# Optimization experiments

Measured on AMD Instinct MI355X. Metric: run time of the kernel, lower is better.

## Reference

```python
import jax, jax.numpy as jnp
import numpy as np

B, L, D = 2, 2048, 2048
HQ, HKV = 32, 8
HD = D // HQ  # 64
ROPE_BASE = 10000.0
ROPE_SCALE = 1.0


def setup_inputs() -> dict:
    key = jax.random.key(0)
    ks = jax.random.split(key, 5)
    s = 0.02
    return {
        "x": jax.random.normal(ks[0], (B, L, D), dtype=jnp.float32),
        "pos_ids": jnp.arange(L, dtype=jnp.int64) if jax.config.jax_enable_x64 else jnp.arange(L, dtype=jnp.int32),
        "wq": jax.random.normal(ks[1], (D, D), dtype=jnp.float32) * s,
        "wk": jax.random.normal(ks[2], (HKV * HD, D), dtype=jnp.float32) * s,
        "wv": jax.random.normal(ks[3], (HKV * HD, D), dtype=jnp.float32) * s,
        "wo": jax.random.normal(ks[4], (D, D), dtype=jnp.float32) * s,
    }


def _rope_cos_sin(pos_ids, rot_dim, dtype):
    half = rot_dim // 2
    idx = jnp.arange(half, dtype=jnp.float32)
    inv_freq = (1.0 / (ROPE_BASE ** (idx / half))) * ROPE_SCALE  # [half]
    freqs = pos_ids.astype(dtype)[:, None] * inv_freq.astype(dtype)[None, :]  # [L, half]
    return jnp.cos(freqs), jnp.sin(freqs)


def _apply_rotary(x, cos, sin):
    # x: [B, L, H, Hd]; interleaved pair rotation on full head dim
    b, l, h, hd = x.shape
    xp = x.reshape(b, l, h, hd // 2, 2)
    x1, x2 = xp[..., 0], xp[..., 1]
    c = cos.reshape(1, l, 1, hd // 2)
    s = sin.reshape(1, l, 1, hd // 2)
    y1 = x1 * c - x2 * s
    y2 = x1 * s + x2 * c
    return jnp.stack([y1, y2], axis=-1).reshape(b, l, h, hd)


def reference(x, pos_ids, wq, wk, wv, wo):
    b, l, d = x.shape
    q = (x @ wq.T).reshape(b, l, HQ, HD)
    k = (x @ wk.T).reshape(b, l, HKV, HD)
    v = (x @ wv.T).reshape(b, l, HKV, HD)

    cos, sin = _rope_cos_sin(pos_ids, HD, x.dtype)
    q = _apply_rotary(q, cos, sin)
    k = _apply_rotary(k, cos, sin)

    group = HQ // HKV  # GQA: each kv head serves `group` consecutive q heads
    k = jnp.repeat(k, group, axis=2)  # [b, l, HQ, HD]
    v = jnp.repeat(v, group, axis=2)

    scale = 1.0 / jnp.sqrt(jnp.asarray(HD, dtype=x.dtype))
    scores = jnp.einsum("bqhd,bkhd->bhqk", q, k) * scale  # [b, HQ, l, l]
    causal = jnp.tril(jnp.ones((l, l), dtype=bool))
    neg = jnp.asarray(jnp.finfo(x.dtype).min, dtype=x.dtype)
    scores = jnp.where(causal[None, None], scores, neg)
    attn = jax.nn.softmax(scores, axis=-1)
    out = jnp.einsum("bhqk,bkhd->bqhd", attn, v).reshape(b, l, d)
    return out @ wo.T
```

## Files before the change

### kernel.cpp

```cpp
#include <hip/hip_runtime.h>
#include <stdint.h>

typedef unsigned short u16;
typedef unsigned int   u32;
typedef __bf16 bf16_t;
typedef bf16_t bf16x8 __attribute__((ext_vector_type(8)));
typedef u16    u16x8  __attribute__((ext_vector_type(8)));
typedef float  f32x4  __attribute__((ext_vector_type(4)));
typedef float  f32x16 __attribute__((ext_vector_type(16)));

#define NB   2
#define NL   2048
#define ND   2048
#define NHQ  32
#define NHKV 8
#define NHD  64
#define NQKV 3072
#define QSCALE 0.18033688011112042f
#define SM_SHIFT 24.0f

__device__ __forceinline__ u16 f2bf(float x){
  union{float f;u32 u;} v; v.f = x;
  u32 r = v.u + 0x7FFFu + ((v.u >> 16) & 1u);
  return (u16)(r >> 16);
}
__device__ __forceinline__ float bf2f(u16 b){
  union{u32 u;float f;} v; v.u = ((u32)b) << 16; return v.f;
}

__device__ __forceinline__ float exp2_hw(float x){
#if __has_builtin(__builtin_amdgcn_exp2f)
  return __builtin_amdgcn_exp2f(x);
#else
  float r; asm("v_exp_f32 %0, %1" : "=v"(r) : "v"(x)); return r;
#endif
}

__device__ __forceinline__ void gload_lds16(const void* g, void* l){
  auto gp = reinterpret_cast<__attribute__((address_space(1))) u16*>(
      (uintptr_t)g);
  auto lp = reinterpret_cast<__attribute__((address_space(3))) u16*>(
      (uintptr_t)l);
  __builtin_amdgcn_global_load_lds(gp, lp, 16, 0, 0);
}

__device__ __forceinline__ f32x4 mfma16(bf16x8 a, bf16x8 b, f32x4 c){
  return __builtin_amdgcn_mfma_f32_16x16x32_bf16(a, b, c, 0, 0, 0);
}
__device__ __forceinline__ f32x16 mfma32(bf16x8 a, bf16x8 b, f32x16 c){
  return __builtin_amdgcn_mfma_f32_32x32x16_bf16(a, b, c, 0, 0, 0);
}
__device__ __forceinline__ u32 cvtpk(float lo, float hi){
  u32 w;
  asm("v_cvt_pk_bf16_f32 %0, %1, %2" : "=v"(w) : "v"(lo), "v"(hi));
  return w;
}

template<int N> __device__ __forceinline__ void lgkm_wait(){
  if      constexpr (N == 0)  asm volatile("s_waitcnt lgkmcnt(0)"  ::: "memory");
  else if constexpr (N == 4)  asm volatile("s_waitcnt lgkmcnt(4)"  ::: "memory");
  else if constexpr (N == 8)  asm volatile("s_waitcnt lgkmcnt(8)"  ::: "memory");
  else if constexpr (N == 12) asm volatile("s_waitcnt lgkmcnt(12)" ::: "memory");
  else if constexpr (N == 14) asm volatile("s_waitcnt lgkmcnt(14)" ::: "memory");
  else                        asm volatile("s_waitcnt lgkmcnt(15)" ::: "memory");
  __builtin_amdgcn_sched_barrier(0);
}

#define CV_S1 2097152
#define CV_S2 3145728
#define CV_S3 3407872
#define CV_S4 3670016
#define CV_S5 4718592
#define CV_TOT (CV_S5 + 65536)

__global__ void k_prep(const float* __restrict__ x,  const float* __restrict__ wq,
                       const float* __restrict__ wk, const float* __restrict__ wv,
                       const float* __restrict__ wo, const int* __restrict__ pos,
                       u16* __restrict__ xb, u16* __restrict__ wqkvb, u16* __restrict__ wob,
                       float* __restrict__ cosT, float* __restrict__ sinT){
  int i = blockIdx.x * 256 + threadIdx.x;
  if (i < CV_S5){
    const float4* src; ushort4* dst; int off;
    if (i < CV_S1)      { src = (const float4*)x;  dst = (ushort4*)xb;    off = i; }
    else if (i < CV_S2) { src = (const float4*)wq; dst = (ushort4*)wqkvb; off = i - CV_S1; }
    else if (i < CV_S3) { src = (const float4*)wk; dst = (ushort4*)wqkvb + 1048576; off = i - CV_S2; }
    else if (i < CV_S4) { src = (const float4*)wv; dst = (ushort4*)wqkvb + 1310720; off = i - CV_S3; }
    else                { src = (const float4*)wo; dst = (ushort4*)wob;   off = i - CV_S4; }
    float4 f = src[off];
    ushort4 o;
    o.x = f2bf(f.x); o.y = f2bf(f.y); o.z = f2bf(f.z); o.w = f2bf(f.w);
    dst[off] = o;
  } else {
    int idx = i - CV_S5;
    int l = idx >> 5, k = idx & 31;
    float p = (float)pos[l];
    float inv = __expf(-((float)k * (1.0f/32.0f)) * 9.210340371976184f);
    float fr = p * inv;
    cosT[idx] = cosf(fr);
    sinT[idx] = sinf(fr);
  }
}

template<int BM, int BN, int WRITE_F32>
__global__ __launch_bounds__(512) void k_gemm9(const u16* __restrict__ A,
                                               const u16* __restrict__ Bm,
                                               void* __restrict__ Cp,
                                               int M, int N, int K){
  constexpr int LA_N = BM/64;
  constexpr int LB_N = BN/64;
  constexpr int LN   = LA_N + LB_N;
  constexpr int MR   = BM/32;
  constexpr int MH   = MR/2;
  constexpr int NF   = BN/64;
  __shared__ u16 LAb[2][BM*64];
  __shared__ u16 LBb[2][BN*64];
  const int tid = threadIdx.x;
  const int lane = tid & 63, w = tid >> 6;
  const int wr = w >> 2, wc = w & 3;
  const int lr = lane & 15, lg = lane >> 4;
  const int tn = blockIdx.x * BN, tm = blockIdx.y * BM;
  const size_t Kb = (size_t)K * 2;
  const char* Ab = (const char*)A;
  const char* Bb = (const char*)Bm;

  u32 soff[LN]; int ldoff[LN];
#pragma unroll
  for (int l = 0; l < LN; ++l){
    int o = ((l < LA_N) ? l : (l - LA_N))*8192 + tid*16;
    int s = o ^ (((o>>7)&7)<<4);
    int row = s >> 7, col = s & 127;
    int trow = (l < LA_N) ? (tm + row) : (tn + row);
    soff[l]  = (u32)((size_t)trow * Kb + col);
    ldoff[l] = o;
  }
  const int c0 = ( lg      ^ (lr & 7)) << 4;
  const int c1 = ((4 + lg) ^ (lr & 7)) << 4;
  const int arow = (wr*(BM/2) + lr) * 128;
  const int brow = (wc*(BN/4) + lr) * 128;

  f32x4 acc[MR][NF] = {};
  bf16x8 bfA[NF][2], bfB[NF][2], afA[MH][2], afB[MH][2];
  const int NT = K >> 6;

#pragma unroll
  for (int l = 0; l < LN; ++l){
    char* base = (l < LA_N) ? (char*)LAb[0] : (char*)LBb[0];
    const char* gb = (l < LA_N) ? Ab : Bb;
    gload_lds16(gb + soff[l], base + ldoff[l]);
  }
  asm volatile("s_waitcnt vmcnt(0)" ::: "memory");
  __builtin_amdgcn_s_barrier();
#pragma unroll
  for (int n = 0; n < NF; ++n){
    bfA[n][0] = *(const bf16x8*)((const char*)LBb[0] + brow + n*2048 + c0);
    bfA[n][1] = *(const bf16x8*)((const char*)LBb[0] + brow + n*2048 + c1);
  }
#pragma unroll
  for (int q = 0; q < MH; ++q){
    afA[q][0] = *(const bf16x8*)((const char*)LAb[0] + arow + q*2048 + c0);
    afA[q][1] = *(const bf16x8*)((const char*)LAb[0] + arow + q*2048 + c1);
  }

#define TILE(laC, laN, lbN, bfc, bfn, PRE, KOFF)                            \
    {                                                                       \
                            \
      _Pragma("unroll")                                                     \
      for (int q = 0; q < MH; ++q){                                         \
        afB[q][0] = *(const bf16x8*)((const char*)(laC) + arow + (MH+q)*2048 + c0); \
        afB[q][1] = *(const bf16x8*)((const char*)(laC) + arow + (MH+q)*2048 + c1); \
      }                                                                     \
      if (PRE){                                                             \
        _Pragma("unroll")                                                   \
        for (int l = 0; l < LN; ++l){                                       \
          char* nb_ = (l < LA_N) ? (char*)(laN) : (char*)(lbN);             \
          const char* gb_ = (l < LA_N) ? Ab : Bb;                           \
          gload_lds16(gb_ + soff[l] + (KOFF), nb_ + ldoff[l]);              \
        }                                                                   \
      }                                                                     \
      lgkm_wait<2*MH>();                                                    \
      __builtin_amdgcn_s_setprio(1);                                        \
      _Pragma("unroll")                                                     \
      for (int q = 0; q < MH; ++q){                                         \
        _Pragma("unroll")                                                   \
        for (int n = 0; n < NF; ++n){                                       \
          acc[q][n] = mfma16(afA[q][0], bfc[n][0], acc[q][n]);              \
          acc[q][n] = mfma16(afA[q][1], bfc[n][1], acc[q][n]);              \
        }                                                                   \
      }                                                                     \
      __builtin_amdgcn_s_setprio(0);                                        \
      asm volatile("s_waitcnt vmcnt(0)" ::: "memory");                      \
      __builtin_amdgcn_s_barrier();                                         \
                        \
      if (PRE){                                                             \
        _Pragma("unroll")                                                   \
        for (int n = 0; n < NF; ++n){                                       \
          bfn[n][0] = *(const bf16x8*)((const char*)(lbN) + brow + n*2048 + c0); \
          bfn[n][1] = *(const bf16x8*)((const char*)(lbN) + brow + n*2048 + c1); \
        }                                                                   \
        _Pragma("unroll")                                                   \
        for (int q = 0; q < MH; ++q){                                       \
          afA[q][0] = *(const bf16x8*)((const char*)(laN) + arow + q*2048 + c0); \
          afA[q][1] = *(const bf16x8*)((const char*)(laN) + arow + q*2048 + c1); \
        }                                                                   \
        lgkm_wait<2*NF + 2*MH>();                                           \
      } else {                                                              \
        lgkm_wait<0>();                                                     \
      }                                                                     \
      __builtin_amdgcn_s_setprio(1);                                        \
      _Pragma("unroll")                                                     \
      for (int q = 0; q < MH; ++q){                                         \
        _Pragma("unroll")                                                   \
        for (int n = 0; n < NF; ++n){                                       \
          acc[MH+q][n] = mfma16(afB[q][0], bfc[n][0], acc[MH+q][n]);        \
          acc[MH+q][n] = mfma16(afB[q][1], bfc[n][1], acc[MH+q][n]);        \
        }                                                                   \
      }                                                                     \
      __builtin_amdgcn_s_setprio(0);                                        \
      __builtin_amdgcn_s_barrier();                                         \
    }

#pragma unroll 1
  for (int kt = 0; kt < NT; kt += 2){
    const bool pre1 = (kt + 2 < NT);
    TILE(LAb[0], LAb[1], LBb[1], bfA, bfB, true, (u32)(kt+1)*128)
    TILE(LAb[1], LAb[0], LBb[0], bfB, bfA, pre1, (u32)(kt+2)*128)
  }
#undef TILE

  const int rb = tm + wr*(BM/2) + lg*4;
  const int cb = tn + wc*(BN/4) + lr;
#pragma unroll
  for (int m = 0; m < MR; ++m){
#pragma unroll
    for (int n = 0; n < NF; ++n){
#pragma unroll
      for (int r = 0; r < 4; ++r){
        size_t off = (size_t)(rb + m*16 + r) * N + (cb + n*16);
        if (WRITE_F32) ((float*)Cp)[off] = acc[m][n][r];
        else           ((u16*)Cp)[off]   = f2bf(acc[m][n][r]);
      }
    }
  }
}

__global__ void k_rope_scatter(const u16* __restrict__ qkv, const float* __restrict__ cosT,
                               const float* __restrict__ sinT,
                               u16* __restrict__ Q, u16* __restrict__ Ko, u16* __restrict__ V){
  const int row = blockIdx.x;
  const int b = row >> 11, l = row & 2047;
  const int t = threadIdx.x;
#pragma unroll
  for (int it = 0; it < 6; ++it){
    int pp = t + it*256;
    u32 xin = *reinterpret_cast<const u32*>(&qkv[(size_t)row*NQKV + pp*2]);
    float x1 = bf2f((u16)(xin & 0xFFFFu));
    float x2 = bf2f((u16)(xin >> 16));
    if (pp < 1280){
      int i = pp & 31;
      float c = cosT[l*32 + i], s = sinT[l*32 + i];
      float y1 = x1*c - x2*s;
      float y2 = x1*s + x2*c;
      if (pp < 1024){
        int hh = pp >> 5, d = (pp & 31)*2;
        u32 o = (u32)f2bf(y1*QSCALE) | ((u32)f2bf(y2*QSCALE) << 16);
        *reinterpret_cast<u32*>(&Q[(((size_t)(b*NHQ + hh))*NL + l)*NHD + d]) = o;
      } else {
        int idx = pp - 1024, kvh = idx >> 5, d = (idx & 31)*2;
        u32 o = (u32)f2bf(y1) | ((u32)f2bf(y2) << 16);
        *reinterpret_cast<u32*>(&Ko[(((size_t)(b*NHKV + kvh))*NL + l)*NHD + d]) = o;
      }
    } else {
      int idx = pp - 1280, kvh = idx >> 5, d = (idx & 31)*2;
      *reinterpret_cast<u32*>(&V[(((size_t)(b*NHKV + kvh))*NL + l)*NHD + d]) = xin;
    }
  }
}

__global__ __launch_bounds__(256) void k_transpose(const u16* __restrict__ V, u16* __restrict__ VT){
  __shared__ u16 T[64*72];
  const int bid = blockIdx.x;
  const int slice = bid >> 5, tile = bid & 31;
  const u16* src = V  + (size_t)slice*NL*NHD + (size_t)tile*64*NHD;
  u16*       dst = VT + (size_t)slice*NHD*NL + (size_t)tile*64;
  const int t = threadIdx.x;
  {
    int r = t >> 2, c0 = (t & 3)*16;
    const u16x8* s = reinterpret_cast<const u16x8*>(src + (size_t)r*NHD + c0);
    *reinterpret_cast<u16x8*>(&T[r*72 + c0])     = s[0];
    *reinterpret_cast<u16x8*>(&T[r*72 + c0 + 8]) = s[1];
  }
  __syncthreads();
  {
    int d = t >> 2, l0 = (t & 3)*16;
    u16x8 v0, v1;
#pragma unroll
    for (int j = 0; j < 8; ++j) v0[j] = T[(l0+j)*72 + d];
#pragma unroll
    for (int j = 0; j < 8; ++j) v1[j] = T[(l0+8+j)*72 + d];
    u16* dp = dst + (size_t)d*NL + l0;
    *reinterpret_cast<u16x8*>(dp)     = v0;
    *reinterpret_cast<u16x8*>(dp + 8) = v1;
  }
}

__device__ __forceinline__ void stage_kv32(const u16* __restrict__ Kp, const u16* __restrict__ VTp,
                                           int kvb, u16* lk, u16* lv, int w, int lane){
  const char* ks = (const char*)(Kp + (size_t)kvb*NHD);
  const char* vs = (const char*)VTp + (size_t)kvb*2;
  const int o = w*1024 + lane*16;
  const int swk = o ^ (((o>>7)&7)<<4);
  gload_lds16(ks + swk, (char*)lk + w*1024);
  const int row = o >> 6, c = o & 63;
  gload_lds16(vs + (size_t)row*(NL*2) + (c ^ (((row>>1)&3)<<4)), (char*)lv + w*1024);
}
__device__ __forceinline__ bf16x8 ldsK(const u16* base, int row, int colb){
  return *reinterpret_cast<const bf16x8*>((const char*)base + row*128 + (colb ^ ((row&7)<<4)));
}
__device__ __forceinline__ bf16x8 ldsV(const u16* base, int row, int colb){
  return *reinterpret_cast<const bf16x8*>((const char*)base + row*64 + (colb ^ (((row>>1)&3)<<4)));
}

__global__ __launch_bounds__(256) void k_attn7(const u16* __restrict__ Q, const u16* __restrict__ Kg,
                                               const u16* __restrict__ VT, u16* __restrict__ O){
  __shared__ u16 LK[2][2048];
  __shared__ u16 LV[2][2048];
  const int tid = threadIdx.x, lane = tid & 63, w = tid >> 6;
  const int q32 = lane & 31, hi = lane >> 5;
  const int f = blockIdx.x;
  const int round = f >> 8, c = f & 255;
  const int i16 = c >> 4;
  const int qti = round*16 + ((round & 1) ? (15 - i16) : i16);
  const int qt = 63 - qti;
  const int grp = c & 15;
  const int b = grp >> 3, kvh = grp & 7;
  const int h = kvh*4 + w;
  const u16* Qp  = Q  + ((size_t)(b*NHQ  + h  ))*NL*NHD;
  const u16* Kp  = Kg + ((size_t)(b*NHKV + kvh))*NL*NHD;
  const u16* VTp = VT + ((size_t)(b*NHKV + kvh))*NHD*NL;

  const int qrow = qt*32 + q32;
  const int ntw  = qt + 1;

  bf16x8 qf[4];
#pragma unroll
  for (int ks = 0; ks < 4; ++ks)
    qf[ks] = *reinterpret_cast<const bf16x8*>(&Qp[(size_t)qrow*NHD + ks*16 + hi*8]);

  f32x16 o0 = {}, o1 = {};
  float lsum = 0.0f;

  stage_kv32(Kp, VTp, 0, LK[0], LV[0], w, lane);
  __syncthreads();

#pragma unroll 1
  for (int j = 0; j < ntw; ++j){
    const int cur = j & 1;
    const u16* lk = LK[cur];
    const u16* lv = LV[cur];
    if (j + 1 < ntw)
      stage_kv32(Kp, VTp, (j+1) << 5, LK[cur^1], LV[cur^1], w, lane);

    const int kvb = j << 5;
    bf16x8 kf[4];
#pragma unroll
    for (int ks = 0; ks < 4; ++ks)
      kf[ks] = ldsK(lk, q32, ks*32 + hi*16);
    f32x16 s0 = {};
    __builtin_amdgcn_s_setprio(1);
#pragma unroll
    for (int ks = 0; ks < 4; ++ks)
      s0 = mfma32(kf[ks], qf[ks], s0);
    __builtin_amdgcn_s_setprio(0);
    if (j == ntw - 1){
#pragma unroll
      for (int r = 0; r < 16; ++r){
        const int kl = (r&3) + 8*(r>>2) + 4*hi;
        if (kvb + kl > qrow) s0[r] = -1e30f;
      }
    }
#pragma unroll
    for (int r = 0; r < 16; ++r) s0[r] = exp2_hw(s0[r] - SM_SHIFT);
    float u[8];
#pragma unroll
    for (int r = 0; r < 8; ++r)  u[r] = s0[r] + s0[r+8];
#pragma unroll
    for (int r = 0; r < 4; ++r)  u[r] += u[r+4];
    lsum += (u[0]+u[1]) + (u[2]+u[3]);
    u32 wds[8];
#pragma unroll
    for (int i = 0; i < 8; ++i) wds[i] = cvtpk(s0[2*i], s0[2*i+1]);
    bf16x8 pf[2];
#pragma unroll
    for (int fi = 0; fi < 2; ++fi){
      u32 x  = wds[4*fi+0], y  = wds[4*fi+2];
      u32 x2 = wds[4*fi+1], y2 = wds[4*fi+3];
      asm("v_permlane32_swap_b32 %0, %1" : "+v"(x),  "+v"(y));
      asm("v_permlane32_swap_b32 %0, %1" : "+v"(x2), "+v"(y2));
      union { u32 wq[4]; bf16x8 v; } uu;
      uu.wq[0] = x; uu.wq[1] = x2; uu.wq[2] = y; uu.wq[3] = y2;
      pf[fi] = uu.v;
    }
    bf16x8 vf[4];
    vf[0] = ldsV(lv, q32,      hi*16);
    vf[1] = ldsV(lv, q32,      32 + hi*16);
    vf[2] = ldsV(lv, 32 + q32, hi*16);
    vf[3] = ldsV(lv, 32 + q32, 32 + hi*16);
    __builtin_amdgcn_s_setprio(1);
    o0 = mfma32(vf[0], pf[0], o0);
    o0 = mfma32(vf[1], pf[1], o0);
    o1 = mfma32(vf[2], pf[0], o1);
    o1 = mfma32(vf[3], pf[1], o1);
    __builtin_amdgcn_s_setprio(0);
    __syncthreads();
  }

  float lt = lsum + __shfl_xor(lsum, 32);
  const float inv = 1.0f / lt;
  u16* Op = O + ((size_t)(b*NL + qrow))*ND + h*NHD;
#pragma unroll
  for (int md = 0; md < 2; ++md){
#pragma unroll
    for (int q4 = 0; q4 < 4; ++q4){
      ushort4 sv;
      float a0 = (md ? o1[4*q4+0] : o0[4*q4+0]) * inv;
      float a1 = (md ? o1[4*q4+1] : o0[4*q4+1]) * inv;
      float a2 = (md ? o1[4*q4+2] : o0[4*q4+2]) * inv;
      float a3 = (md ? o1[4*q4+3] : o0[4*q4+3]) * inv;
      sv.x = f2bf(a0); sv.y = f2bf(a1); sv.z = f2bf(a2); sv.w = f2bf(a3);
      *reinterpret_cast<ushort4*>(&Op[md*32 + 8*q4 + 4*hi]) = sv;
    }
  }
}

extern "C" void kernel_launch(void* const* d_in, const int* in_sizes, int n_in,
                              void* d_out, int out_size, void* d_ws, size_t ws_size,
                              hipStream_t stream){
  (void)in_sizes; (void)n_in; (void)out_size; (void)ws_size;
  const float* x   = (const float*)d_in[0];
  const int*   pos = (const int*)  d_in[1];
  const float* wq  = (const float*)d_in[2];
  const float* wk  = (const float*)d_in[3];
  const float* wv  = (const float*)d_in[4];
  const float* wo  = (const float*)d_in[5];

  char* ws = (char*)d_ws;
  size_t off = 0;
  auto alloc = [&](size_t bytes) -> void* {
    void* p = ws + off;
    off += (bytes + 255) & ~(size_t)255;
    return p;
  };
  const size_t n_x   = (size_t)NB*NL*ND;
  const size_t n_wq  = (size_t)ND*ND;

  u16* xb    = (u16*)alloc(n_x*2);
  u16* wqkvb = (u16*)alloc((size_t)NQKV*ND*2);
  u16* wob   = (u16*)alloc(n_wq*2);
  u16* qkv   = (u16*)alloc((size_t)NB*NL*NQKV*2);
  u16* Qb    = (u16*)alloc((size_t)NB*NHQ*NL*NHD*2);
  u16* Kb    = (u16*)alloc((size_t)NB*NHKV*NL*NHD*2);
  u16* Vb    = (u16*)alloc((size_t)NB*NHKV*NL*NHD*2);
  u16* VTb   = (u16*)alloc((size_t)NB*NHKV*NHD*NL*2);
  float* cosT= (float*)alloc((size_t)NL*32*4);
  float* sinT= (float*)alloc((size_t)NL*32*4);

  k_prep<<<CV_TOT/256, 256, 0, stream>>>(x, wq, wk, wv, wo, pos, xb, wqkvb, wob, cosT, sinT);

  k_gemm9<256,192,0><<<dim3(NQKV/192, (NB*NL)/256), 512, 0, stream>>>(xb, wqkvb, qkv, NB*NL, NQKV, ND);
  k_rope_scatter<<<NB*NL, 256, 0, stream>>>(qkv, cosT, sinT, Qb, Kb, Vb);
  k_transpose<<<NB*NHKV*(NL/64), 256, 0, stream>>>(Vb, VTb);
  k_attn7<<<1024, 256, 0, stream>>>(Qb, Kb, VTb, xb);
  k_gemm9<128,256,1><<<dim3(ND/256, (NB*NL)/128), 512, 0, stream>>>(xb, wob, d_out, NB*NL, ND, ND);
}
```

Measured before the change: 179.5 us.

## Process 64-key KV tiles per attention iteration and compute row sums via MFMA

The attention kernel now stages and processes 64 keys per loop iteration instead of 32. This halves the number of barriers and loop iterations and gives each wave more independent MFMAs to interleave. The softmax denominator is now accumulated with an extra MFMA against a ones vector, replacing the scalar add/shuffle reduction. The cost is doubled LDS, more registers, and extra masked work on the last tile, since the causal trim is now at 64-key granularity.

```diff
diff --git a/kernel.cpp b/kernel.cpp
--- a/kernel.cpp
+++ b/kernel.cpp
@@ -163,7 +163,6 @@
 
 #define TILE(laC, laN, lbN, bfc, bfn, PRE, KOFF)                            \
     {                                                                       \
-                            \
       _Pragma("unroll")                                                     \
       for (int q = 0; q < MH; ++q){                                         \
         afB[q][0] = *(const bf16x8*)((const char*)(laC) + arow + (MH+q)*2048 + c0); \
@@ -190,7 +189,6 @@
       __builtin_amdgcn_s_setprio(0);                                        \
       asm volatile("s_waitcnt vmcnt(0)" ::: "memory");                      \
       __builtin_amdgcn_s_barrier();                                         \
-                        \
       if (PRE){                                                             \
         _Pragma("unroll")                                                   \
         for (int n = 0; n < NF; ++n){                                       \
@@ -303,27 +301,27 @@
   }
 }
 
-__device__ __forceinline__ void stage_kv32(const u16* __restrict__ Kp, const u16* __restrict__ VTp,
-                                           int kvb, u16* lk, u16* lv, int w, int lane){
+__device__ __forceinline__ void stage_kv64(const u16* __restrict__ Kp, const u16* __restrict__ VTp,
+                                           int kvb, u16* lk, u16* lv, int tid){
   const char* ks = (const char*)(Kp + (size_t)kvb*NHD);
   const char* vs = (const char*)VTp + (size_t)kvb*2;
-  const int o = w*1024 + lane*16;
-  const int swk = o ^ (((o>>7)&7)<<4);
-  gload_lds16(ks + swk, (char*)lk + w*1024);
-  const int row = o >> 6, c = o & 63;
-  gload_lds16(vs + (size_t)row*(NL*2) + (c ^ (((row>>1)&3)<<4)), (char*)lv + w*1024);
-}
-__device__ __forceinline__ bf16x8 ldsK(const u16* base, int row, int colb){
+#pragma unroll
+  for (int i = 0; i < 2; ++i){
+    const int o = tid*16 + i*4096;
+    const int sw = o ^ (((o>>7)&7)<<4);
+    gload_lds16(ks + sw, (char*)lk + o);
+    const int row = o >> 7, c = o & 127;
+    gload_lds16(vs + (size_t)row*(NL*2) + (c ^ ((row&7)<<4)), (char*)lv + o);
+  }
+}
+__device__ __forceinline__ bf16x8 lds128(const u16* base, int row, int colb){
   return *reinterpret_cast<const bf16x8*>((const char*)base + row*128 + (colb ^ ((row&7)<<4)));
 }
-__device__ __forceinline__ bf16x8 ldsV(const u16* base, int row, int colb){
-  return *reinterpret_cast<const bf16x8*>((const char*)base + row*64 + (colb ^ (((row>>1)&3)<<4)));
-}
-
-__global__ __launch_bounds__(256) void k_attn7(const u16* __restrict__ Q, const u16* __restrict__ Kg,
+
+__global__ __launch_bounds__(256) void k_attn8(const u16* __restrict__ Q, const u16* __restrict__ Kg,
                                                const u16* __restrict__ VT, u16* __restrict__ O){
-  __shared__ u16 LK[2][2048];
-  __shared__ u16 LV[2][2048];
+  __shared__ u16 LK[2][4096];
+  __shared__ u16 LV[2][4096];
   const int tid = threadIdx.x, lane = tid & 63, w = tid >> 6;
   const int q32 = lane & 31, hi = lane >> 5;
   const int f = blockIdx.x;
@@ -339,83 +337,107 @@
   const u16* VTp = VT + ((size_t)(b*NHKV + kvh))*NHD*NL;
 
   const int qrow = qt*32 + q32;
-  const int ntw  = qt + 1;
+  const int nt   = (qt >> 1) + 1;
 
   bf16x8 qf[4];
 #pragma unroll
   for (int ks = 0; ks < 4; ++ks)
     qf[ks] = *reinterpret_cast<const bf16x8*>(&Qp[(size_t)qrow*NHD + ks*16 + hi*8]);
 
-  f32x16 o0 = {}, o1 = {};
-  float lsum = 0.0f;
-
-  stage_kv32(Kp, VTp, 0, LK[0], LV[0], w, lane);
+  bf16x8 onef;
+  {
+    union { u32 wd[4]; bf16x8 v; } uu;
+#pragma unroll
+    for (int i = 0; i < 4; ++i) uu.wd[i] = 0x3F803F80u;
+    onef = uu.v;
+  }
+
+  f32x16 o0 = {}, o1 = {}, ls = {};
+
+  stage_kv64(Kp, VTp, 0, LK[0], LV[0], tid);
   __syncthreads();
 
 #pragma unroll 1
-  for (int j = 0; j < ntw; ++j){
+  for (int j = 0; j < nt; ++j){
     const int cur = j & 1;
     const u16* lk = LK[cur];
     const u16* lv = LV[cur];
-    if (j + 1 < ntw)
-      stage_kv32(Kp, VTp, (j+1) << 5, LK[cur^1], LV[cur^1], w, lane);
-
-    const int kvb = j << 5;
-    bf16x8 kf[4];
-#pragma unroll
-    for (int ks = 0; ks < 4; ++ks)
-      kf[ks] = ldsK(lk, q32, ks*32 + hi*16);
-    f32x16 s0 = {};
+    if (j + 1 < nt)
+      stage_kv64(Kp, VTp, (j+1) << 6, LK[cur^1], LV[cur^1], tid);
+
+    const int kvb = j << 6;
+    bf16x8 kf0[4], kf1[4];
+#pragma unroll
+    for (int ks = 0; ks < 4; ++ks){
+      kf0[ks] = lds128(lk, q32,      ks*32 + hi*16);
+      kf1[ks] = lds128(lk, 32 + q32, ks*32 + hi*16);
+    }
+    f32x16 s0 = {}, s1 = {};
     __builtin_amdgcn_s_setprio(1);
 #pragma unroll
-    for (int ks = 0; ks < 4; ++ks)
-      s0 = mfma32(kf[ks], qf[ks], s0);
+    for (int ks = 0; ks < 4; ++ks){
+      s0 = mfma32(kf0[ks], qf[ks], s0);
+      s1 = mfma32(kf1[ks], qf[ks], s1);
+    }
     __builtin_amdgcn_s_setprio(0);
-    if (j == ntw - 1){
+    if (j == nt - 1){
 #pragma unroll
       for (int r = 0; r < 16; ++r){
         const int kl = (r&3) + 8*(r>>2) + 4*hi;
-        if (kvb + kl > qrow) s0[r] = -1e30f;
+        if (kvb + kl      > qrow) s0[r] = -1e30f;
+        if (kvb + 32 + kl > qrow) s1[r] = -1e30f;
       }
     }
 #pragma unroll
-    for (int r = 0; r < 16; ++r) s0[r] = exp2_hw(s0[r] - SM_SHIFT);
-    float u[8];
-#pragma unroll
-    for (int r = 0; r < 8; ++r)  u[r] = s0[r] + s0[r+8];
-#pragma unroll
-    for (int r = 0; r < 4; ++r)  u[r] += u[r+4];
-    lsum += (u[0]+u[1]) + (u[2]+u[3]);
-    u32 wds[8];
-#pragma unroll
-    for (int i = 0; i < 8; ++i) wds[i] = cvtpk(s0[2*i], s0[2*i+1]);
-    bf16x8 pf[2];
+    for (int r = 0; r < 16; ++r){
+      s0[r] = exp2_hw(s0[r] - SM_SHIFT);
+      s1[r] = exp2_hw(s1[r] - SM_SHIFT);
+    }
+    u32 wd0[8], wd1[8];
+#pragma unroll
+    for (int i = 0; i < 8; ++i){
+      wd0[i] = cvtpk(s0[2*i], s0[2*i+1]);
+      wd1[i] = cvtpk(s1[2*i], s1[2*i+1]);
+    }
+    bf16x8 pf[4];
 #pragma unroll
     for (int fi = 0; fi < 2; ++fi){
-      u32 x  = wds[4*fi+0], y  = wds[4*fi+2];
-      u32 x2 = wds[4*fi+1], y2 = wds[4*fi+3];
+      u32 x  = wd0[4*fi+0], y  = wd0[4*fi+2];
+      u32 x2 = wd0[4*fi+1], y2 = wd0[4*fi+3];
       asm("v_permlane32_swap_b32 %0, %1" : "+v"(x),  "+v"(y));
       asm("v_permlane32_swap_b32 %0, %1" : "+v"(x2), "+v"(y2));
       union { u32 wq[4]; bf16x8 v; } uu;
       uu.wq[0] = x; uu.wq[1] = x2; uu.wq[2] = y; uu.wq[3] = y2;
       pf[fi] = uu.v;
     }
-    bf16x8 vf[4];
-    vf[0] = ldsV(lv, q32,      hi*16);
-    vf[1] = ldsV(lv, q32,      32 + hi*16);
-    vf[2] = ldsV(lv, 32 + q32, hi*16);
-    vf[3] = ldsV(lv, 32 + q32, 32 + hi*16);
+#pragma unroll
+    for (int fi = 0; fi < 2; ++fi){
+      u32 x  = wd1[4*fi+0], y  = wd1[4*fi+2];
+      u32 x2 = wd1[4*fi+1], y2 = wd1[4*fi+3];
+      asm("v_permlane32_swap_b32 %0, %1" : "+v"(x),  "+v"(y));
+      asm("v_permlane32_swap_b32 %0, %1" : "+v"(x2), "+v"(y2));
+      union { u32 wq[4]; bf16x8 v; } uu;
+      uu.wq[0] = x; uu.wq[1] = x2; uu.wq[2] = y; uu.wq[3] = y2;
+      pf[2+fi] = uu.v;
+    }
+    bf16x8 vf0[4], vf1[4];
+#pragma unroll
+    for (int ks = 0; ks < 4; ++ks){
+      vf0[ks] = lds128(lv, q32,      ks*32 + hi*16);
+      vf1[ks] = lds128(lv, 32 + q32, ks*32 + hi*16);
+    }
     __builtin_amdgcn_s_setprio(1);
-    o0 = mfma32(vf[0], pf[0], o0);
-    o0 = mfma32(vf[1], pf[1], o0);
-    o1 = mfma32(vf[2], pf[0], o1);
-    o1 = mfma32(vf[3], pf[1], o1);
+#pragma unroll
+    for (int ks = 0; ks < 4; ++ks){
+      o0 = mfma32(vf0[ks], pf[ks], o0);
+      o1 = mfma32(vf1[ks], pf[ks], o1);
+      ls = mfma32(onef,    pf[ks], ls);
+    }
     __builtin_amdgcn_s_setprio(0);
     __syncthreads();
   }
 
-  float lt = lsum + __shfl_xor(lsum, 32);
-  const float inv = 1.0f / lt;
+  const float inv = 1.0f / ls[0];
   u16* Op = O + ((size_t)(b*NL + qrow))*ND + h*NHD;
 #pragma unroll
   for (int md = 0; md < 2; ++md){
@@ -469,6 +491,6 @@
   k_gemm9<256,192,0><<<dim3(NQKV/192, (NB*NL)/256), 512, 0, stream>>>(xb, wqkvb, qkv, NB*NL, NQKV, ND);
   k_rope_scatter<<<NB*NL, 256, 0, stream>>>(qkv, cosT, sinT, Qb, Kb, Vb);
   k_transpose<<<NB*NHKV*(NL/64), 256, 0, stream>>>(Vb, VTb);
-  k_attn7<<<1024, 256, 0, stream>>>(Qb, Kb, VTb, xb);
+  k_attn8<<<1024, 256, 0, stream>>>(Qb, Kb, VTb, xb);
   k_gemm9<128,256,1><<<dim3(ND/256, (NB*NL)/128), 512, 0, stream>>>(xb, wob, d_out, NB*NL, ND, ND);
 }
```

Measured after the change: 188.4 us. 4.9% more time.
